# Kernel tuning notes

Hardware: AMD Instinct MI355X
Metric: run time of the kernel (lower is better)

## Reference

```python
import jax, jax.numpy as jnp
import numpy as np

B, U = 64, 512          # batch, max_units
CORE, UNIT = 512, 256   # core_output_size, unit_embedding_size
HID, ACT = 1024, 12     # hidden_layer_size, ACTION_COUNT


def setup_inputs() -> dict:
    key = jax.random.key(0)
    ks = jax.random.split(key, 6)
    core_output = jax.random.normal(ks[0], (B, 1, CORE), dtype=jnp.float32)
    own_unit_embeddings = jax.random.normal(ks[1], (B, U, UNIT), dtype=jnp.float32)
    nr_units = jax.random.randint(ks[2], (B, 1), 0, U, dtype=jnp.int32)
    nr_own_flags = jax.random.randint(ks[3], (B, 1), 0, 64, dtype=jnp.int32)
    W1 = jax.random.normal(ks[4], (CORE + UNIT, HID), dtype=jnp.float32) * (1.0 / np.sqrt(CORE + UNIT))
    b1 = jnp.zeros((HID,), dtype=jnp.float32)
    W2 = jax.random.normal(ks[5], (HID, ACT), dtype=jnp.float32) * (1.0 / np.sqrt(HID))
    b2 = jnp.zeros((ACT,), dtype=jnp.float32)
    return {"core_output": core_output, "own_unit_embeddings": own_unit_embeddings,
            "nr_units": nr_units, "nr_own_flags": nr_own_flags,
            "W1": W1, "b1": b1, "W2": W2, "b2": b2}


def reference(core_output, own_unit_embeddings, nr_units, nr_own_flags, W1, b1, W2, b2):
    b, u, _ = own_unit_embeddings.shape
    # broadcast core output to every unit slot and concat along features: [B, U, UNIT+CORE]
    core_rep = jnp.broadcast_to(core_output, (b, u, core_output.shape[-1]))
    combined = jnp.concatenate([own_unit_embeddings, core_rep], axis=-1)
    autoregressive_embedding = jax.nn.relu(jnp.einsum('buf,fh->buh', combined, W1) + b1)
    logits = jnp.einsum('buh,ha->bua', autoregressive_embedding, W2) + b2
    action_probs = jax.nn.softmax(logits, axis=-1)
    # vectorized range mask: mask[i, f:n, :] = 1 else 1e-9
    idx = jnp.arange(u, dtype=nr_units.dtype)[None, :]        # [1, U]
    valid = (idx >= nr_own_flags) & (idx < nr_units)          # [B, U]
    mask = jnp.where(valid, 1.0, 1e-9).astype(action_probs.dtype)[:, :, None]
    return action_probs * mask, autoregressive_embedding
```

## Files before the change

kernel.cpp:

```cpp
#include <hip/hip_runtime.h>
#include <hip/hip_fp16.h>
#include <cstdint>

typedef unsigned short ushort_t;
typedef _Float16 f16x8 __attribute__((ext_vector_type(8)));
typedef float f32x4 __attribute__((ext_vector_type(4)));
typedef unsigned int u32x4 __attribute__((ext_vector_type(4)));

#define M_TOT  32768
#define K_EMB  256
#define K_CORE 512
#define ACT    12

__device__ __forceinline__ unsigned int pack2h(float a, float b) {
    __half2 h = __floats2half2_rn(a, b);
    union { __half2 h2; unsigned int u; } v; v.h2 = h; return v.u;
}

__global__ __launch_bounds__(256) void transpose_k(const float* __restrict__ W1,
                                                   ushort_t* __restrict__ W1T) {
    __shared__ float tile[64][65];
    const int t = threadIdx.x;
    const int k0 = blockIdx.x * 64, n0 = blockIdx.y * 64;
    const int r = t >> 4, c4 = (t & 15) * 4;
#pragma unroll
    for (int p = 0; p < 4; ++p) {
        const int row = r + p * 16;
        const float4 v = *(const float4*)(W1 + (size_t)(k0 + row) * 1024 + n0 + c4);
        tile[row][c4 + 0] = v.x; tile[row][c4 + 1] = v.y;
        tile[row][c4 + 2] = v.z; tile[row][c4 + 3] = v.w;
    }
    __syncthreads();
#pragma unroll
    for (int p = 0; p < 4; ++p) {
        const int nrow = r + p * 16;
        uint2 o;
        o.x = pack2h(tile[c4 + 0][nrow], tile[c4 + 1][nrow]);
        o.y = pack2h(tile[c4 + 2][nrow], tile[c4 + 3][nrow]);
        *(uint2*)(W1T + (size_t)(n0 + nrow) * 256 + k0 + c4) = o;
    }
}

__global__ __launch_bounds__(256) void corepart_k(const float* __restrict__ core,
                                                  const float* __restrict__ W1,
                                                  const float* __restrict__ b1,
                                                  float* __restrict__ cp) {
    const int b = blockIdx.y;
    const int n = blockIdx.x * 256 + threadIdx.x;
    const float* cr = core + b * K_CORE;
    const float* wp = W1 + (size_t)K_EMB * 1024 + n;
    float s0 = 0.f, s1 = 0.f, s2 = 0.f, s3 = 0.f;
#pragma unroll 4
    for (int k = 0; k < K_CORE; k += 4) {
        s0 += cr[k + 0] * wp[(size_t)(k + 0) * 1024];
        s1 += cr[k + 1] * wp[(size_t)(k + 1) * 1024];
        s2 += cr[k + 2] * wp[(size_t)(k + 2) * 1024];
        s3 += cr[k + 3] * wp[(size_t)(k + 3) * 1024];
    }
    cp[b * 1024 + n] = b1[n] + ((s0 + s1) + (s2 + s3));
}

__global__ __launch_bounds__(256, 2) void fused_k(const float* __restrict__ emb,
                                                  const ushort_t* __restrict__ w1t,
                                                  const float* __restrict__ cp,
                                                  const float* __restrict__ W2,
                                                  const float* __restrict__ b2,
                                                  const int* __restrict__ nr_units,
                                                  const int* __restrict__ nr_flags,
                                                  float* __restrict__ out0,
                                                  float* __restrict__ out1) {
    __shared__ __align__(16) ushort_t Asl[64 * 256];
    __shared__ __align__(16) ushort_t Bsl[2][128 * 32];
    __shared__ __align__(16) float logitAcc[4][64][ACT];

    const int t = threadIdx.x;
    const int w = t >> 6, L = t & 63;
    const int lane16 = L & 15, qd = L >> 4;
    const int m0 = blockIdx.x * 64;
    const int bb = blockIdx.x >> 3;

    {
        const int g = t & 31;
        const int rsub = t >> 5;
#pragma unroll
        for (int p = 0; p < 8; ++p) {
            const int r = p * 8 + rsub;
            const float* src = emb + (size_t)(m0 + r) * K_EMB + g * 8;
            const f32x4 v0 = __builtin_nontemporal_load((const f32x4*)src);
            const f32x4 v1 = __builtin_nontemporal_load((const f32x4*)src + 1);
            u32x4 pk;
            pk[0] = pack2h(v0[0], v0[1]); pk[1] = pack2h(v0[2], v0[3]);
            pk[2] = pack2h(v1[0], v1[1]); pk[3] = pack2h(v1[2], v1[3]);
            *(u32x4*)((char*)Asl + r * 512 + ((g ^ (r & 7)) << 4)) = pk;
        }
    }

    const int rB = t >> 2, gB = t & 3;
    const ushort_t* gBa = w1t + (size_t)rB * K_EMB + gB * 8;
    const int wb0 = rB * 64 + ((gB ^ ((rB >> 1) & 3)) << 4);
    const int wb1 = wb0 + 64 * 64;

    {
        const u32x4 b0 = *(const u32x4*)gBa;
        const u32x4 b1v = *(const u32x4*)(gBa + 64 * K_EMB);
        *(u32x4*)((char*)Bsl + wb0) = b0;
        *(u32x4*)((char*)Bsl + wb1) = b1v;
    }
    __syncthreads();

    const int araw = lane16 * 512;
    const int axor = lane16 & 7;
    const int bswz = (qd ^ ((lane16 >> 1) & 3)) << 4;
    int boffc[2];
#pragma unroll
    for (int ni = 0; ni < 2; ++ni)
        boffc[ni] = (w * 32 + ni * 16 + lane16) * 64 + bswz;

    f32x4 acc[2][4];
#pragma unroll
    for (int ni = 0; ni < 2; ++ni)
#pragma unroll
        for (int mi = 0; mi < 4; ++mi) acc[ni][mi] = (f32x4){0.f, 0.f, 0.f, 0.f};
    f32x4 la[4][3];
#pragma unroll
    for (int mi = 0; mi < 4; ++mi)
#pragma unroll
        for (int c = 0; c < 3; ++c) la[mi][c] = (f32x4){0.f, 0.f, 0.f, 0.f};

    u32x4 pb0, pb1;
    int cur = 0;
    for (int it = 0; it < 64; ++it) {
        const int ks = it & 7;
        if (it < 63) {
            const int itn = it + 1;
            const size_t off = (size_t)(itn >> 3) * 128 * K_EMB + (size_t)(itn & 7) * 32;
            pb0 = *(const u32x4*)(gBa + off);
            pb1 = *(const u32x4*)(gBa + 64 * K_EMB + off);
        }
        const int ga = (((ks << 2) | qd) ^ axor) << 4;
        f16x8 af[4], bf[2];
#pragma unroll
        for (int mi = 0; mi < 4; ++mi)
            af[mi] = *(const f16x8*)((const char*)Asl + mi * 8192 + araw + ga);
        const char* bbase = (const char*)Bsl + cur * 8192;
#pragma unroll
        for (int ni = 0; ni < 2; ++ni)
            bf[ni] = *(const f16x8*)(bbase + boffc[ni]);
#pragma unroll
        for (int ni = 0; ni < 2; ++ni)
#pragma unroll
            for (int mi = 0; mi < 4; ++mi)
                acc[ni][mi] = __builtin_amdgcn_mfma_f32_16x16x32_f16(bf[ni], af[mi], acc[ni][mi], 0, 0, 0);

        if ((it & 7) == 7) {
            const int nt = it >> 3;
#pragma unroll
            for (int ni = 0; ni < 2; ++ni) {
                const int nbase = nt * 128 + w * 32 + ni * 16 + qd * 4;
                const f32x4 cpv = *(const f32x4*)(cp + bb * 1024 + nbase);
#pragma unroll
                for (int mi = 0; mi < 4; ++mi) {
                    f32x4 v = acc[ni][mi] + cpv;
#pragma unroll
                    for (int j = 0; j < 4; ++j) v[j] = v[j] > 0.f ? v[j] : 0.f;
                    acc[ni][mi] = v;
                    const size_t m = (size_t)(m0 + mi * 16 + lane16);
                    __builtin_nontemporal_store(v, (f32x4*)(out1 + m * 1024 + nbase));
                }
#pragma unroll
                for (int r = 0; r < 4; ++r) {
                    const f32x4* wp = (const f32x4*)(W2 + (size_t)(nbase + r) * ACT);
                    const f32x4 w2a = wp[0], w2b = wp[1], w2c = wp[2];
#pragma unroll
                    for (int mi = 0; mi < 4; ++mi) {
                        const float vv = acc[ni][mi][r];
                        la[mi][0] += w2a * vv;
                        la[mi][1] += w2b * vv;
                        la[mi][2] += w2c * vv;
                    }
                }
#pragma unroll
                for (int mi = 0; mi < 4; ++mi) acc[ni][mi] = (f32x4){0.f, 0.f, 0.f, 0.f};
            }
        }

        if (it < 63) {
            char* bnxt = (char*)Bsl + ((cur ^ 1) * 8192);
            *(u32x4*)(bnxt + wb0) = pb0;
            *(u32x4*)(bnxt + wb1) = pb1;
        }
        __syncthreads();
        cur ^= 1;
    }

#pragma unroll
    for (int mi = 0; mi < 4; ++mi)
#pragma unroll
        for (int c = 0; c < 3; ++c)
#pragma unroll
            for (int j = 0; j < 4; ++j) {
                la[mi][c][j] += __shfl_xor(la[mi][c][j], 16, 64);
                la[mi][c][j] += __shfl_xor(la[mi][c][j], 32, 64);
            }
    if (L < 16) {
#pragma unroll
        for (int mi = 0; mi < 4; ++mi) {
            f32x4* p = (f32x4*)&logitAcc[w][mi * 16 + L][0];
            p[0] = la[mi][0]; p[1] = la[mi][1]; p[2] = la[mi][2];
        }
    }
    __syncthreads();

    if (t < 64) {
        float lg[ACT];
#pragma unroll
        for (int a = 0; a < ACT; ++a)
            lg[a] = logitAcc[0][t][a] + logitAcc[1][t][a]
                  + logitAcc[2][t][a] + logitAcc[3][t][a] + b2[a];
        float mx = lg[0];
#pragma unroll
        for (int a = 1; a < ACT; ++a) mx = fmaxf(mx, lg[a]);
        float s = 0.f;
#pragma unroll
        for (int a = 0; a < ACT; ++a) { lg[a] = __expf(lg[a] - mx); s += lg[a]; }
        const float inv = 1.f / s;
        const int m = m0 + t;
        const int u = m & 511;
        const float msk = (u >= nr_flags[bb] && u < nr_units[bb]) ? 1.0f : 1e-9f;
        f32x4 o0, o1, o2;
#pragma unroll
        for (int j = 0; j < 4; ++j) {
            o0[j] = lg[j] * inv * msk;
            o1[j] = lg[j + 4] * inv * msk;
            o2[j] = lg[j + 8] * inv * msk;
        }
        f32x4* op = (f32x4*)(out0 + (size_t)m * ACT);
        __builtin_nontemporal_store(o0, op + 0);
        __builtin_nontemporal_store(o1, op + 1);
        __builtin_nontemporal_store(o2, op + 2);
    }
}

extern "C" void kernel_launch(void* const* d_in, const int* in_sizes, int n_in,
                              void* d_out, int out_size, void* d_ws, size_t ws_size,
                              hipStream_t stream) {
    const float* core   = (const float*)d_in[0];
    const float* emb    = (const float*)d_in[1];
    const int* nr_units = (const int*)d_in[2];
    const int* nr_flags = (const int*)d_in[3];
    const float* W1     = (const float*)d_in[4];
    const float* b1     = (const float*)d_in[5];
    const float* W2     = (const float*)d_in[6];
    const float* b2     = (const float*)d_in[7];

    float* out0 = (float*)d_out;
    float* out1 = out0 + (size_t)M_TOT * ACT;

    ushort_t* w1t = (ushort_t*)d_ws;
    float* cp = (float*)((char*)d_ws + (size_t)1024 * 256 * 2);

    transpose_k<<<dim3(4, 16), 256, 0, stream>>>(W1, w1t);
    corepart_k<<<dim3(4, 64), 256, 0, stream>>>(core, W1, b1, cp);
    fused_k<<<dim3(512), 256, 0, stream>>>(emb, w1t, cp, W2, b2, nr_units, nr_flags, out0, out1);
}
```

Measured before the change: 243.1 us.

## Merge prep kernels, split core GEMV over K, shrink LDS for occupancy

Merges the W1 transpose and the core-projection kernels into one 1024-thread launch. The core GEMV is split four ways along K, and the partial sums are reduced through shared memory. The aim is to cut one launch and add parallelism to the latency-bound prologue. In the fused kernel, the per-wave logit buffers become a single shared buffer filled with LDS atomicAdd, and launch bounds are raised to 3 blocks per CU. This trades atomic contention in LDS for lower LDS use and higher occupancy, and register pressure may rise as a risk.

```diff
diff --git a/kernel.cpp b/kernel.cpp
--- a/kernel.cpp
+++ b/kernel.cpp
@@ -17,50 +17,51 @@
     union { __half2 h2; unsigned int u; } v; v.h2 = h; return v.u;
 }
 
-__global__ __launch_bounds__(256) void transpose_k(const float* __restrict__ W1,
-                                                   ushort_t* __restrict__ W1T) {
+__global__ __launch_bounds__(1024) void prep_k(const float* __restrict__ W1,
+                                               ushort_t* __restrict__ W1T,
+                                               const float* __restrict__ core,
+                                               const float* __restrict__ b1,
+                                               float* __restrict__ cp) {
     __shared__ float tile[64][65];
+    __shared__ float part[3][256];
+    const int id = blockIdx.x;
     const int t = threadIdx.x;
-    const int k0 = blockIdx.x * 64, n0 = blockIdx.y * 64;
-    const int r = t >> 4, c4 = (t & 15) * 4;
-#pragma unroll
-    for (int p = 0; p < 4; ++p) {
-        const int row = r + p * 16;
-        const float4 v = *(const float4*)(W1 + (size_t)(k0 + row) * 1024 + n0 + c4);
-        tile[row][c4 + 0] = v.x; tile[row][c4 + 1] = v.y;
-        tile[row][c4 + 2] = v.z; tile[row][c4 + 3] = v.w;
-    }
-    __syncthreads();
-#pragma unroll
-    for (int p = 0; p < 4; ++p) {
-        const int nrow = r + p * 16;
+    if (id < 64) {
+        const int k0 = (id & 3) * 64, n0 = (id >> 2) * 64;
+        const int r = t >> 4, c4 = (t & 15) * 4;
+        const float4 v = *(const float4*)(W1 + (size_t)(k0 + r) * 1024 + n0 + c4);
+        tile[r][c4 + 0] = v.x; tile[r][c4 + 1] = v.y;
+        tile[r][c4 + 2] = v.z; tile[r][c4 + 3] = v.w;
+        __syncthreads();
         uint2 o;
-        o.x = pack2h(tile[c4 + 0][nrow], tile[c4 + 1][nrow]);
-        o.y = pack2h(tile[c4 + 2][nrow], tile[c4 + 3][nrow]);
-        *(uint2*)(W1T + (size_t)(n0 + nrow) * 256 + k0 + c4) = o;
-    }
-}
-
-__global__ __launch_bounds__(256) void corepart_k(const float* __restrict__ core,
-                                                  const float* __restrict__ W1,
-                                                  const float* __restrict__ b1,
-                                                  float* __restrict__ cp) {
-    const int b = blockIdx.y;
-    const int n = blockIdx.x * 256 + threadIdx.x;
-    const float* cr = core + b * K_CORE;
-    const float* wp = W1 + (size_t)K_EMB * 1024 + n;
-    float s0 = 0.f, s1 = 0.f, s2 = 0.f, s3 = 0.f;
-#pragma unroll 4
-    for (int k = 0; k < K_CORE; k += 4) {
-        s0 += cr[k + 0] * wp[(size_t)(k + 0) * 1024];
-        s1 += cr[k + 1] * wp[(size_t)(k + 1) * 1024];
-        s2 += cr[k + 2] * wp[(size_t)(k + 2) * 1024];
-        s3 += cr[k + 3] * wp[(size_t)(k + 3) * 1024];
-    }
-    cp[b * 1024 + n] = b1[n] + ((s0 + s1) + (s2 + s3));
-}
-
-__global__ __launch_bounds__(256, 2) void fused_k(const float* __restrict__ emb,
+        o.x = pack2h(tile[c4 + 0][r], tile[c4 + 1][r]);
+        o.y = pack2h(tile[c4 + 2][r], tile[c4 + 3][r]);
+        *(uint2*)(W1T + (size_t)(n0 + r) * 256 + k0 + c4) = o;
+    } else {
+        const int xb = id - 64;
+        const int b = xb >> 2;
+        const int nl = t & 255;
+        const int n = (xb & 3) * 256 + nl;
+        const int kq = t >> 8;
+        const float* cr = core + (size_t)b * K_CORE + kq * 128;
+        const float* wp = W1 + (size_t)(K_EMB + kq * 128) * 1024 + n;
+        float s0 = 0.f, s1 = 0.f, s2 = 0.f, s3 = 0.f;
+#pragma unroll 8
+        for (int k = 0; k < 128; k += 4) {
+            s0 += cr[k + 0] * wp[(size_t)(k + 0) * 1024];
+            s1 += cr[k + 1] * wp[(size_t)(k + 1) * 1024];
+            s2 += cr[k + 2] * wp[(size_t)(k + 2) * 1024];
+            s3 += cr[k + 3] * wp[(size_t)(k + 3) * 1024];
+        }
+        const float s = (s0 + s1) + (s2 + s3);
+        if (kq) part[kq - 1][nl] = s;
+        __syncthreads();
+        if (kq == 0)
+            cp[b * 1024 + n] = b1[n] + s + part[0][nl] + part[1][nl] + part[2][nl];
+    }
+}
+
+__global__ __launch_bounds__(256, 3) void fused_k(const float* __restrict__ emb,
                                                   const ushort_t* __restrict__ w1t,
                                                   const float* __restrict__ cp,
                                                   const float* __restrict__ W2,
@@ -71,13 +72,15 @@
                                                   float* __restrict__ out1) {
     __shared__ __align__(16) ushort_t Asl[64 * 256];
     __shared__ __align__(16) ushort_t Bsl[2][128 * 32];
-    __shared__ __align__(16) float logitAcc[4][64][ACT];
+    __shared__ __align__(16) float logitAcc[64][ACT];
 
     const int t = threadIdx.x;
     const int w = t >> 6, L = t & 63;
     const int lane16 = L & 15, qd = L >> 4;
     const int m0 = blockIdx.x * 64;
     const int bb = blockIdx.x >> 3;
+
+    if (t < 192) ((f32x4*)logitAcc)[t] = (f32x4){0.f, 0.f, 0.f, 0.f};
 
     {
         const int g = t & 31;
@@ -205,8 +208,12 @@
     if (L < 16) {
 #pragma unroll
         for (int mi = 0; mi < 4; ++mi) {
-            f32x4* p = (f32x4*)&logitAcc[w][mi * 16 + L][0];
-            p[0] = la[mi][0]; p[1] = la[mi][1]; p[2] = la[mi][2];
+            const int row = mi * 16 + L;
+#pragma unroll
+            for (int c = 0; c < 3; ++c)
+#pragma unroll
+                for (int j = 0; j < 4; ++j)
+                    atomicAdd(&logitAcc[row][c * 4 + j], la[mi][c][j]);
         }
     }
     __syncthreads();
@@ -214,9 +221,7 @@
     if (t < 64) {
         float lg[ACT];
 #pragma unroll
-        for (int a = 0; a < ACT; ++a)
-            lg[a] = logitAcc[0][t][a] + logitAcc[1][t][a]
-                  + logitAcc[2][t][a] + logitAcc[3][t][a] + b2[a];
+        for (int a = 0; a < ACT; ++a) lg[a] = logitAcc[t][a] + b2[a];
         float mx = lg[0];
 #pragma unroll
         for (int a = 1; a < ACT; ++a) mx = fmaxf(mx, lg[a]);
@@ -259,7 +264,6 @@
     ushort_t* w1t = (ushort_t*)d_ws;
     float* cp = (float*)((char*)d_ws + (size_t)1024 * 256 * 2);
 
-    transpose_k<<<dim3(4, 16), 256, 0, stream>>>(W1, w1t);
-    corepart_k<<<dim3(4, 64), 256, 0, stream>>>(core, W1, b1, cp);
+    prep_k<<<dim3(320), 1024, 0, stream>>>(W1, w1t, core, b1, cp);
     fused_k<<<dim3(512), 256, 0, stream>>>(emb, w1t, cp, W2, b2, nr_units, nr_flags, out0, out1);
 }
```

After: 256.9 us. 1.06x slower.
